# Kernel tuning notes

Hardware: AMD Instinct MI355X
Metric: run time of the kernel (lower is better)

Reference implementation:

```python
import jax, jax.numpy as jnp
import numpy as np

N = 100000      # nodes
E = 1250000     # edges
D_IN = 64
D_OUT = 64


def _gconv(x, src, dst, W_rel, W_root, b, n_nodes):
    # PyG GraphConv (aggr='add'): out = lin_rel(sum_{j in N(i)} x_j) + lin_root(x_i)
    agg = jax.ops.segment_sum(x[src], dst, num_segments=n_nodes)  # [N, d]
    return agg @ W_rel + b + x @ W_root


def setup_inputs() -> dict:
    key = jax.random.key(0)
    ks = jax.random.split(key, 12)
    graph = jax.random.normal(ks[0], (N, D_IN), dtype=jnp.float32)
    edge_index = jax.random.randint(ks[1], (2, E), 0, N, dtype=jnp.int32)
    s_in = 1.0 / np.sqrt(D_IN)
    s_out = 1.0 / np.sqrt(D_OUT)
    d = {
        "graph": graph,
        "edge_index": edge_index,
        "W1_rel": jax.random.uniform(ks[2], (D_IN, D_OUT), jnp.float32, -s_in, s_in),
        "W1_root": jax.random.uniform(ks[3], (D_IN, D_OUT), jnp.float32, -s_in, s_in),
        "b1": jnp.zeros((D_OUT,), jnp.float32),
        "W2_rel": jax.random.uniform(ks[4], (D_OUT, D_OUT), jnp.float32, -s_out, s_out),
        "W2_root": jax.random.uniform(ks[5], (D_OUT, D_OUT), jnp.float32, -s_out, s_out),
        "b2": jnp.zeros((D_OUT,), jnp.float32),
        "W3_rel": jax.random.uniform(ks[6], (D_OUT, D_OUT), jnp.float32, -s_out, s_out),
        "W3_root": jax.random.uniform(ks[7], (D_OUT, D_OUT), jnp.float32, -s_out, s_out),
        "b3": jnp.zeros((D_OUT,), jnp.float32),
    }
    return d


def reference(graph, edge_index, W1_rel, W1_root, b1, W2_rel, W2_root, b2, W3_rel, W3_root, b3):
    src, dst = edge_index[0], edge_index[1]
    n = graph.shape[0]
    y1 = jax.nn.elu(_gconv(graph, src, dst, W1_rel, W1_root, b1, n))
    y2 = jax.nn.elu(_gconv(y1, src, dst, W2_rel, W2_root, b2, n))
    y3 = jax.nn.sigmoid(_gconv(y2, src, dst, W3_rel, W3_root, b3, n))
    return (y1, y2, y3)
```

## Files before the change

kernel.cpp:

```cpp
#include <hip/hip_runtime.h>
#include <hip/hip_bf16.h>
#include <math.h>


#define D 64
#define BSHIFT 9
#define BW 512
#define BCAP 8192

typedef __attribute__((ext_vector_type(8))) short short8;
typedef __attribute__((ext_vector_type(4))) float f32x4;

__device__ __forceinline__ ushort f2b(float f) {
    uint x = __float_as_uint(f);
    uint r = (x + 0x7fffu + ((x >> 16) & 1u)) >> 16;
    return (ushort)r;
}
__device__ __forceinline__ float b2f(ushort u) {
    return __uint_as_float(((uint)u) << 16);
}


__global__ __launch_bounds__(256) void convert_w(const float* __restrict__ w0,
                                                 const float* __restrict__ w1,
                                                 const float* __restrict__ w2,
                                                 const float* __restrict__ w3,
                                                 const float* __restrict__ w4,
                                                 const float* __restrict__ w5,
                                                 ushort* __restrict__ out) {
    int m = blockIdx.x >> 4;
    int t = (blockIdx.x & 15) * 256 + threadIdx.x;
    const float* src = m == 0 ? w0 : m == 1 ? w1 : m == 2 ? w2 : m == 3 ? w3 : m == 4 ? w4 : w5;
    int k = t >> 6, d = t & 63;
    out[m * 4096 + d * 64 + k] = f2b(src[t]);
}


__global__ __launch_bounds__(1024) void bucket_scatter(const int* __restrict__ src,
                                                       const int* __restrict__ dst,
                                                       int* __restrict__ bucketCnt,
                                                       unsigned long long* __restrict__ store,
                                                       int E) {
    __shared__ int h[256], base[256], cur[256];
    int t = threadIdx.x;
    if (t < 256) { h[t] = 0; cur[t] = 0; }
    __syncthreads();
    int e = blockIdx.x * 1024 + t;
    int s = 0, d = 0, b = 0;
    bool ok = e < E;
    if (ok) {
        s = src[e];
        d = dst[e];
        b = d >> BSHIFT;
        atomicAdd(&h[b], 1);
    }
    __syncthreads();
    if (t < 256) base[t] = h[t] ? atomicAdd(&bucketCnt[t], h[t]) : 0;
    __syncthreads();
    if (ok) {
        int r = atomicAdd(&cur[b], 1);
        int pos = base[b] + r;
        if (pos < BCAP)
            store[(size_t)b * BCAP + pos] = ((unsigned long long)(uint)d << 32) | (uint)s;
    }
}


__global__ __launch_bounds__(256) void scan_buckets(const int* __restrict__ bucketCnt,
                                                    int* __restrict__ bucketBase,
                                                    int* __restrict__ offs,
                                                    int nb, int n, int E) {
    __shared__ int tmp[256];
    int t = threadIdx.x;
    int v = (t < nb) ? bucketCnt[t] : 0;
    tmp[t] = v;
    __syncthreads();
    for (int off = 1; off < 256; off <<= 1) {
        int add = (t >= off) ? tmp[t - off] : 0;
        __syncthreads();
        tmp[t] += add;
        __syncthreads();
    }
    if (t < nb) bucketBase[t] = tmp[t] - v;
    if (t == 0) offs[n] = E;
}


__global__ __launch_bounds__(1024) void bucket_build(const int* __restrict__ bucketCnt,
                                                     const int* __restrict__ bucketBase,
                                                     const unsigned long long* __restrict__ store,
                                                     int* __restrict__ offs,
                                                     int* __restrict__ src_sorted, int n) {
    __shared__ int h[BW], loc[BW], cur[BW];
    __shared__ unsigned long long se[BCAP];
    int b = blockIdx.x, t = threadIdx.x;
    int cnt = bucketCnt[b];
    if (cnt > BCAP) cnt = BCAP;
    int obase = bucketBase[b];
    int d0 = b << BSHIFT;
    int nd = n - d0;
    if (nd > BW) nd = BW;
    if (t < BW) { h[t] = 0; cur[t] = 0; }
    __syncthreads();
    for (int i = t; i < cnt; i += 1024) {
        unsigned long long p = store[(size_t)b * BCAP + i];
        se[i] = p;
        atomicAdd(&h[(int)(p >> 32) - d0], 1);
    }
    __syncthreads();
    if (t < BW) loc[t] = h[t];
    __syncthreads();
    for (int off = 1; off < BW; off <<= 1) {
        int add = (t < BW && t >= off) ? loc[t - off] : 0;
        __syncthreads();
        if (t < BW) loc[t] += add;
        __syncthreads();
    }
    if (t < nd) offs[d0 + t] = obase + loc[t] - h[t];
    __syncthreads();
    for (int i = t; i < cnt; i += 1024) {
        unsigned long long p = se[i];
        int dl = (int)(p >> 32) - d0;
        int r = atomicAdd(&cur[dl], 1);
        src_sorted[obase + loc[dl] - h[dl] + r] = (int)(p & 0xffffffffULL);
    }
}


__global__ __launch_bounds__(256) void gemm_ro(const float* __restrict__ x,
                                               const ushort* __restrict__ WtR,
                                               const ushort* __restrict__ WtO,
                                               const float* __restrict__ bias,
                                               ushort* __restrict__ hrel,
                                               ushort* __restrict__ hroot, int n) {
    __shared__ ushort hsR[4][16 * 64];
    __shared__ ushort hsO[4][16 * 64];
    int t = threadIdx.x;
    int w = t >> 6, l = t & 63;
    int i0 = blockIdx.x * 64 + w * 16;
    int lr = l & 15, kb = l >> 4;
    int row = i0 + lr;
    int rowc = row < n ? row : n - 1;

    short8 a[2];
#pragma unroll
    for (int s = 0; s < 2; ++s) {
        const float* p = x + (size_t)rowc * D + s * 32 + kb * 8;
        float4 u = *(const float4*)p;
        float4 v = *(const float4*)(p + 4);
        a[s][0] = f2b(u.x); a[s][1] = f2b(u.y); a[s][2] = f2b(u.z); a[s][3] = f2b(u.w);
        a[s][4] = f2b(v.x); a[s][5] = f2b(v.y); a[s][6] = f2b(v.z); a[s][7] = f2b(v.w);
    }

#pragma unroll
    for (int ct = 0; ct < 4; ++ct) {
        f32x4 accR = (f32x4){0.f, 0.f, 0.f, 0.f};
        f32x4 accO = (f32x4){0.f, 0.f, 0.f, 0.f};
#pragma unroll
        for (int s = 0; s < 2; ++s) {
            short8 bR = *(const short8*)(WtR + (ct * 16 + lr) * D + s * 32 + kb * 8);
            short8 bO = *(const short8*)(WtO + (ct * 16 + lr) * D + s * 32 + kb * 8);
            accR = __builtin_amdgcn_mfma_f32_16x16x32_bf16(a[s], bR, accR, 0, 0, 0);
            accO = __builtin_amdgcn_mfma_f32_16x16x32_bf16(a[s], bO, accO, 0, 0, 0);
        }
        float bv = bias[ct * 16 + lr];
#pragma unroll
        for (int i = 0; i < 4; ++i) {
            hsR[w][(kb * 4 + i) * 64 + ct * 16 + lr] = f2b(accR[i]);
            hsO[w][(kb * 4 + i) * 64 + ct * 16 + lr] = f2b(accO[i] + bv);
        }
    }
    __syncthreads();

    int r = l >> 2, ch = l & 3;
    int grow = i0 + r;
    if (grow < n) {
        const ushort* spR = &hsR[w][r * 64 + ch * 16];
        const ushort* spO = &hsO[w][r * 64 + ch * 16];
        float4 r0 = *(const float4*)spR;
        float4 r1 = *(const float4*)(spR + 8);
        float4 o0 = *(const float4*)spO;
        float4 o1 = *(const float4*)(spO + 8);
        *(float4*)(hrel + (size_t)grow * D + ch * 16) = r0;
        *(float4*)(hrel + (size_t)grow * D + ch * 16 + 8) = r1;
        *(float4*)(hroot + (size_t)grow * D + ch * 16) = o0;
        *(float4*)(hroot + (size_t)grow * D + ch * 16 + 8) = o1;
    }
}


template <int ACT>
__global__ __launch_bounds__(256) void agg_act(const ushort* __restrict__ hrel,
                                               const ushort* __restrict__ hroot,
                                               const int* __restrict__ offs,
                                               const int* __restrict__ srcs,
                                               float* __restrict__ y, int n) {
    int node = blockIdx.x * 4 + (threadIdx.x >> 6);
    int l = threadIdx.x & 63;
    if (node >= n) return;
    int beg = offs[node];
    int end = offs[node + 1];
    float acc = b2f(hroot[(size_t)node * D + l]);
    for (int e = beg; e < end; e += 8) {
        float v[8];
#pragma unroll
        for (int i = 0; i < 8; ++i) {
            int ee = (e + i < end) ? e + i : end - 1;
            v[i] = b2f(hrel[(size_t)srcs[ee] * D + l]);
        }
#pragma unroll
        for (int i = 1; i < 8; ++i)
            if (e + i >= end) v[i] = 0.f;
        acc += ((v[0] + v[1]) + (v[2] + v[3])) + ((v[4] + v[5]) + (v[6] + v[7]));
    }
    float out;
    if (ACT == 0) out = acc > 0.f ? acc : expf(acc) - 1.f;
    else          out = 1.f / (1.f + expf(-acc));
    y[(size_t)node * D + l] = out;
}


extern "C" void kernel_launch(void* const* d_in, const int* in_sizes, int n_in,
                              void* d_out, int out_size, void* d_ws, size_t ws_size,
                              hipStream_t stream) {
    const float* graph = (const float*)d_in[0];
    const int* eidx    = (const int*)d_in[1];
    const float* W1r = (const float*)d_in[2];
    const float* W1o = (const float*)d_in[3];
    const float* b1  = (const float*)d_in[4];
    const float* W2r = (const float*)d_in[5];
    const float* W2o = (const float*)d_in[6];
    const float* b2  = (const float*)d_in[7];
    const float* W3r = (const float*)d_in[8];
    const float* W3o = (const float*)d_in[9];
    const float* b3  = (const float*)d_in[10];

    int n = in_sizes[0] / D;
    int E = in_sizes[1] / 2;
    const int* src  = eidx;
    const int* dstl = eidx + E;
    int nb = (n + BW - 1) >> BSHIFT;

    char* w = (char*)d_ws;
    auto carve = [&](size_t bytes) {
        void* p = (void*)w;
        w += (bytes + 255) & ~(size_t)255;
        return p;
    };
    ushort* hrel  = (ushort*)carve((size_t)n * D * sizeof(ushort));
    ushort* hroot = (ushort*)carve((size_t)n * D * sizeof(ushort));
    unsigned long long* store = (unsigned long long*)hrel;
    int* offs       = (int*)carve((size_t)(n + 1) * sizeof(int));
    int* src_sorted = (int*)carve((size_t)E * sizeof(int));
    int* bucketCnt  = (int*)carve(256 * sizeof(int));
    int* bucketBase = (int*)carve(256 * sizeof(int));
    ushort* wt      = (ushort*)carve(6 * 4096 * sizeof(ushort));
    ushort* wtR1 = wt;
    ushort* wtO1 = wt + 1 * 4096;
    ushort* wtR2 = wt + 2 * 4096;
    ushort* wtO2 = wt + 3 * 4096;
    ushort* wtR3 = wt + 4 * 4096;
    ushort* wtO3 = wt + 5 * 4096;

    int eb1 = (E + 1023) / 1024;
    int tb  = (n + 63) / 64;
    int ab  = (n + 3) / 4;

    hipMemsetAsync(bucketCnt, 0, 256 * sizeof(int), stream);
    convert_w<<<96, 256, 0, stream>>>(W1r, W1o, W2r, W2o, W3r, W3o, wt);
    bucket_scatter<<<eb1, 1024, 0, stream>>>(src, dstl, bucketCnt, store, E);
    scan_buckets<<<1, 256, 0, stream>>>(bucketCnt, bucketBase, offs, nb, n, E);
    bucket_build<<<nb, 1024, 0, stream>>>(bucketCnt, bucketBase, store, offs, src_sorted, n);

    float* out = (float*)d_out;
    float* y1 = out;
    float* y2 = out + (size_t)n * D;
    float* y3 = out + 2 * (size_t)n * D;

    gemm_ro<<<tb, 256, 0, stream>>>(graph, wtR1, wtO1, b1, hrel, hroot, n);
    agg_act<0><<<ab, 256, 0, stream>>>(hrel, hroot, offs, src_sorted, y1, n);
    gemm_ro<<<tb, 256, 0, stream>>>(y1, wtR2, wtO2, b2, hrel, hroot, n);
    agg_act<0><<<ab, 256, 0, stream>>>(hrel, hroot, offs, src_sorted, y2, n);
    gemm_ro<<<tb, 256, 0, stream>>>(y2, wtR3, wtO3, b3, hrel, hroot, n);
    agg_act<1><<<ab, 256, 0, stream>>>(hrel, hroot, offs, src_sorted, y3, n);
}
```

Baseline: 335.3 us.

## Split aggregation wavefront into four edge groups with 8-byte bf16 loads

Reworks the per-node gather-sum so each 64-lane wavefront handles four edges at once: 16 lanes per edge, each loading four bf16 features as one 8-byte load. Partial sums are combined with cross-lane shuffles, then the root term and activation are applied and one quarter of the lanes write a float4. This is meant to raise memory-level parallelism and cut the number of load instructions in the latency-bound gather. The cost is shuffle reductions and redundant activation math on lanes that never store.

```diff
diff --git a/kernel.cpp b/kernel.cpp
--- a/kernel.cpp
+++ b/kernel.cpp
@@ -198,25 +198,53 @@
     int node = blockIdx.x * 4 + (threadIdx.x >> 6);
     int l = threadIdx.x & 63;
     if (node >= n) return;
+    int q = l >> 4, r = l & 15;
     int beg = offs[node];
     int end = offs[node + 1];
-    float acc = b2f(hroot[(size_t)node * D + l]);
-    for (int e = beg; e < end; e += 8) {
-        float v[8];
-#pragma unroll
-        for (int i = 0; i < 8; ++i) {
-            int ee = (e + i < end) ? e + i : end - 1;
-            v[i] = b2f(hrel[(size_t)srcs[ee] * D + l]);
+
+    float a0 = 0.f, a1 = 0.f, a2 = 0.f, a3 = 0.f;
+    for (int e0 = beg; e0 < end; e0 += 16) {
+#pragma unroll
+        for (int k = 0; k < 4; ++k) {
+            int ee = e0 + k * 4 + q;
+            int eec = ee < end ? ee : end - 1;
+            int s = srcs[eec];
+            uint2 u = *(const uint2*)(hrel + (size_t)s * D + r * 4);
+            float m = (ee < end) ? 1.f : 0.f;
+            a0 = fmaf(__uint_as_float(u.x << 16), m, a0);
+            a1 = fmaf(__uint_as_float(u.x & 0xffff0000u), m, a1);
+            a2 = fmaf(__uint_as_float(u.y << 16), m, a2);
+            a3 = fmaf(__uint_as_float(u.y & 0xffff0000u), m, a3);
         }
-#pragma unroll
-        for (int i = 1; i < 8; ++i)
-            if (e + i >= end) v[i] = 0.f;
-        acc += ((v[0] + v[1]) + (v[2] + v[3])) + ((v[4] + v[5]) + (v[6] + v[7]));
-    }
-    float out;
-    if (ACT == 0) out = acc > 0.f ? acc : expf(acc) - 1.f;
-    else          out = 1.f / (1.f + expf(-acc));
-    y[(size_t)node * D + l] = out;
+    }
+
+    a0 += __shfl_xor(a0, 32); a0 += __shfl_xor(a0, 16);
+    a1 += __shfl_xor(a1, 32); a1 += __shfl_xor(a1, 16);
+    a2 += __shfl_xor(a2, 32); a2 += __shfl_xor(a2, 16);
+    a3 += __shfl_xor(a3, 32); a3 += __shfl_xor(a3, 16);
+
+    uint2 hr = *(const uint2*)(hroot + (size_t)node * D + r * 4);
+    a0 += __uint_as_float(hr.x << 16);
+    a1 += __uint_as_float(hr.x & 0xffff0000u);
+    a2 += __uint_as_float(hr.y << 16);
+    a3 += __uint_as_float(hr.y & 0xffff0000u);
+
+    if (ACT == 0) {
+        a0 = a0 > 0.f ? a0 : expf(a0) - 1.f;
+        a1 = a1 > 0.f ? a1 : expf(a1) - 1.f;
+        a2 = a2 > 0.f ? a2 : expf(a2) - 1.f;
+        a3 = a3 > 0.f ? a3 : expf(a3) - 1.f;
+    } else {
+        a0 = 1.f / (1.f + expf(-a0));
+        a1 = 1.f / (1.f + expf(-a1));
+        a2 = 1.f / (1.f + expf(-a2));
+        a3 = 1.f / (1.f + expf(-a3));
+    }
+
+    if (q == 0) {
+        float4 o; o.x = a0; o.y = a1; o.z = a2; o.w = a3;
+        *(float4*)(y + (size_t)node * D + r * 4) = o;
+    }
 }
 
 
```

Measured after the change: 328.8 us. No clear change (-1.9%).
